# Performance work log

Measured on AMD Instinct MI355X. Metric: run time of the kernel, lower is better.

The kernel has to match this reference:

```python
import jax, jax.numpy as jnp
import numpy as np

B, T, C, H, N = 2, 1024, 2048, 32, 64
KVH = 8                       # GQA kv heads
KV = KVH * N                  # 512
REP = H // KVH                # 4
EPS = 1e-6
LORA = [96, 96, 64, 256, 64]  # xw, xa, xv, xg, xk lora dims


def rmsnorm(x, w, eps=EPS):
    xf = x.astype(jnp.float32)
    var = jnp.mean(xf * xf, axis=-1, keepdims=True)
    return (w * (xf * jax.lax.rsqrt(var + eps))).astype(x.dtype)


def rotate_half(x):
    x1, x2 = jnp.split(x, 2, axis=-1)
    return jnp.concatenate([-x2, x1], axis=-1)


def rwkv7_scan(r, w, k, v, a, b, state0):
    # r,w,k,v,a,b: [B,T,H,N]; state0: [B,H,N,N] (value x key)
    # per step: S = S*exp(w) + (S@a) b^T + v k^T ; o = S @ r
    def step(S, inp):
        r_t, w_t, k_t, v_t, a_t, b_t = inp  # each [B,H,N]
        sa = jnp.einsum('bhvk,bhk->bhv', S, a_t)
        S = (S * jnp.exp(w_t)[:, :, None, :]
             + sa[..., None] * b_t[:, :, None, :]
             + v_t[..., None] * k_t[:, :, None, :])
        o = jnp.einsum('bhvk,bhk->bhv', S, r_t)
        return S, o
    seqs = tuple(jnp.moveaxis(t, 1, 0) for t in (r, w, k, v, a, b))
    S, o = jax.lax.scan(step, state0, seqs)
    return jnp.moveaxis(o, 0, 1), S


def setup_inputs() -> dict:
    key = jax.random.key(0)
    ks = jax.random.split(key, 24)
    g = lambda i, shape, s=0.02: jax.random.normal(ks[i], shape, jnp.float32) * s
    # real rope cache, theta = 1e6, rotary_dim = N
    pos = jnp.arange(T, dtype=jnp.float32)
    inv = 1.0 / (1e6 ** (jnp.arange(0, N, 2, dtype=jnp.float32) / N))
    ang = pos[:, None] * inv[None, :]
    ang = jnp.concatenate([ang, ang], axis=-1)  # [T, N]
    cos = jnp.broadcast_to(jnp.cos(ang)[None], (B, T, N))
    sin = jnp.broadcast_to(jnp.sin(ang)[None], (B, T, N))
    return dict(
        x_in=jax.random.normal(ks[0], (B, T, C), jnp.float32),
        v_first=jax.random.normal(ks[1], (B, T, KVH, N), jnp.float32),
        k_first=jax.random.normal(ks[2], (B, T, KVH, N), jnp.float32),
        state=jnp.zeros((B, H, N, N), jnp.float32),
        calc_cos=cos, calc_sin=sin,
        ln1=jnp.ones((C,), jnp.float32), ln2=jnp.ones((C,), jnp.float32),
        ln_r=jnp.ones((N,), jnp.float32), ln_k=jnp.ones((N,), jnp.float32),
        wavgk1=g(3, (C, sum(LORA))),
        w0=g(4, (H * N,)), w2=g(5, (LORA[0], H * N)),
        a0=g(6, (H * N,)), a2=g(7, (LORA[1], H * N)),
        v0=g(8, (KV,)), v2=g(9, (LORA[2], KV)),
        k0=g(10, (KV,)), k2=g(11, (LORA[4], KV)),
        g2=g(12, (LORA[3], H * N)),
        r_k=g(13, (H, N)),
        RKV_W=g(14, (C, H * N + 2 * KV)),
        O_W=g(15, (H * N, C)),
        R_bias=g(16, (H * N,)), K_bias=g(17, (KV,)), V_bias=g(18, (KV,)),
    )


def _forward(x_in, v_first, k_first, state, calc_cos, calc_sin,
             ln1, ln2, ln_r, ln_k, wavgk1, w0, w2, a0, a2, v0, v2,
             k0, k2, g2, r_k, RKV_W, O_W, R_bias, K_bias, V_bias):
    x = rmsnorm(x_in, ln1)
    xw, xa, xv, xg, xk = jnp.split(x @ wavgk1, np.cumsum(LORA)[:-1].tolist(), axis=-1)
    r, k, v = jnp.split(x @ RKV_W, [H * N, H * N + KV], axis=-1)
    r = (r + R_bias).reshape(B, T, H, N)
    k = (k + K_bias).reshape(B, T, KVH, N)
    v = (v + V_bias).reshape(B, T, KVH, N)
    r = rmsnorm(r, ln_r)
    k = rmsnorm(k, ln_k)
    cos = calc_cos[:, :, None, :]
    sin = calc_sin[:, :, None, :]
    r = r * cos + rotate_half(r) * sin
    k = k * cos + rotate_half(k) * sin
    # layer_id != 0: sigmoid-gated interpolation toward first-layer v/k
    v = v + (v_first - v) * jax.nn.sigmoid(xv @ v2 + v0).reshape(B, T, KVH, N)
    k = k + (k_first - k) * jax.nn.sigmoid(xk @ k2 + k0).reshape(B, T, KVH, N)
    # GQA repeat (contiguous per kv head, as repeat_kv does)
    k = jnp.repeat(k, REP, axis=2).reshape(B, T, H * N)
    v = jnp.repeat(v, REP, axis=2).reshape(B, T, H * N)
    a = jax.nn.sigmoid(xa @ a2 + a0)
    kh = k.reshape(B, T, H, N)
    kk = (kh / (jnp.linalg.norm(kh, axis=-1, keepdims=True) + 1e-12)).reshape(B, T, H * N)
    w = jnp.tanh(xw) @ w2 + w0
    w = -jax.nn.softplus(-w) - 0.5
    k = k * (1.0 - w + a)
    aa = -kk
    bb = kk * a
    wlog = -jnp.exp(w)
    sh = (B, T, H, N)
    o, state = rwkv7_scan(r, wlog.reshape(sh), k.reshape(sh), v.reshape(sh),
                          aa.reshape(sh), bb.reshape(sh), state)
    xx = o.reshape(B, T, H * N) * (float(N) ** -0.5)
    bonus = ((r * k.reshape(sh) * r_k).sum(axis=-1, keepdims=True)
             * v.reshape(sh)).reshape(B, T, H * N)
    xx = xx + bonus
    out = (xx * (jax.nn.sigmoid(xg) @ g2)) @ O_W
    x_res = x_in + out
    output = rmsnorm(x_res, ln2)
    return output, x[:, -1], state, v_first, k_first, x_res


def reference(x_in, v_first, k_first, state, calc_cos, calc_sin,
              ln1, ln2, ln_r, ln_k, wavgk1, w0, w2, a0, a2, v0, v2,
              k0, k2, g2, r_k, RKV_W, O_W, R_bias, K_bias, V_bias):
    return _forward(x_in, v_first, k_first, state, calc_cos, calc_sin,
                    ln1, ln2, ln_r, ln_k, wavgk1, w0, w2, a0, a2, v0, v2,
                    k0, k2, g2, r_k, RKV_W, O_W, R_bias, K_bias, V_bias)
```

## Files before the change

### kernel.cpp

```cpp
#include <hip/hip_runtime.h>
#include <hip/hip_bf16.h>

#define BT 2
#define TT 1024
#define CC 2048
#define HH 32
#define MM (BT*TT)
#define TCH 512
#define NCH (TT/TCH)
#define RECB 896

typedef __attribute__((ext_vector_type(8))) short short8;
typedef __attribute__((ext_vector_type(4))) float floatx4;
typedef __attribute__((ext_vector_type(2))) float f32x2;

static __device__ __forceinline__ float bf2f(__hip_bfloat16 x){ return __bfloat162float(x); }
static __device__ __forceinline__ __hip_bfloat16 f2bf(float x){ return __float2bfloat16(x); }
static __device__ __forceinline__ float sigm(float x){ return 1.0f/(1.0f + expf(-x)); }
static __device__ __forceinline__ float u2f(unsigned short u){
  union { unsigned int i; float f; } x; x.i = ((unsigned int)u) << 16; return x.f;
}
static __device__ __forceinline__ float ulo(unsigned int u){ return __uint_as_float(u << 16); }
static __device__ __forceinline__ float uhi(unsigned int u){ return __uint_as_float(u & 0xffff0000u); }
static __device__ __forceinline__ unsigned short bfbits(float x){
  __hip_bfloat16 h = f2bf(x);
  unsigned short s; __builtin_memcpy(&s, &h, 2); return s;
}
static __device__ __forceinline__ unsigned int pkbf(float lo, float hi){
  return (unsigned int)bfbits(lo) | ((unsigned int)bfbits(hi) << 16);
}

#if defined(__has_builtin)
#if __has_builtin(__builtin_amdgcn_global_load_lds)
#define HAVE_GLL 1
#endif
#endif

#ifdef HAVE_GLL
static __device__ __forceinline__ void gll16(const void* g, void* l){
  __builtin_amdgcn_global_load_lds(
      (__attribute__((address_space(1))) void*)const_cast<void*>(g),
      (__attribute__((address_space(3))) void*)l,
      16, 0, 0);
}
#endif

#define DPP_ADD(x, ctrl) ((x) + __int_as_float(__builtin_amdgcn_update_dpp(0, __float_as_int(x), (ctrl), 0xF, 0xF, true)))

#if defined(__has_builtin)
#if __has_builtin(__builtin_amdgcn_permlane16_swap) && __has_builtin(__builtin_amdgcn_permlane32_swap)
#define HAVE_PLSWAP 1
#endif
#endif

#ifdef HAVE_PLSWAP
typedef unsigned int uint2v __attribute__((ext_vector_type(2)));
static __device__ __forceinline__ float row16_pair_add(float x){
  unsigned int u = __float_as_uint(x);
  uint2v r = __builtin_amdgcn_permlane16_swap(u, u, false, false);
  return __uint_as_float(r[0]) + __uint_as_float(r[1]);
}
static __device__ __forceinline__ float half32_pair_add(float x){
  unsigned int u = __float_as_uint(x);
  uint2v r = __builtin_amdgcn_permlane32_swap(u, u, false, false);
  return __uint_as_float(r[0]) + __uint_as_float(r[1]);
}
#else
static __device__ __forceinline__ float row16_pair_add(float x){ return x + __shfl_xor(x, 16); }
static __device__ __forceinline__ float half32_pair_add(float x){ return x + __shfl_xor(x, 32); }
#endif

static __device__ __forceinline__ float red8(float x){
  x = DPP_ADD(x, 0xB1);
  x = DPP_ADD(x, 0x4E);
  x = DPP_ADD(x, 0x141);
  return x;
}
static __device__ __forceinline__ float red32(float x){
  x = DPP_ADD(x, 0xB1);
  x = DPP_ADD(x, 0x4E);
  x = DPP_ADD(x, 0x124);
  x = DPP_ADD(x, 0x128);
  return row16_pair_add(x);
}
static __device__ __forceinline__ float red64(float x){
  x = DPP_ADD(x, 0xB1);
  x = DPP_ADD(x, 0x4E);
  x = DPP_ADD(x, 0x124);
  x = DPP_ADD(x, 0x128);
  x = row16_pair_add(x);
  return half32_pair_add(x);
}

__global__ __launch_bounds__(256) void tcvt_kernel(
    const float* __restrict__ W, __hip_bfloat16* __restrict__ Wt,
    int K, int N, int Npad)
{
  __shared__ float tile[32][33];
  const int bn = blockIdx.x*32, bk = blockIdx.y*32;
  const int tx = threadIdx.x & 31, ty0 = threadIdx.x >> 5;
#pragma unroll
  for (int i=0;i<4;++i){
    const int kk = bk + ty0 + i*8;
    float val = 0.f;
    if (kk < K && bn + tx < N) val = W[(size_t)kk*N + bn + tx];
    tile[ty0 + i*8][tx] = val;
  }
  __syncthreads();
#pragma unroll
  for (int i=0;i<4;++i){
    const int nn = bn + ty0 + i*8;
    const int kk = bk + tx;
    if (nn < Npad && kk < K) Wt[(size_t)nn*K + kk] = f2bf(tile[tx][ty0 + i*8]);
  }
}

__global__ __launch_bounds__(256) void rmsnorm1_kernel(
    const float* __restrict__ x_in,
    const float* __restrict__ ln1,
    __hip_bfloat16* __restrict__ x_bf,
    float* __restrict__ x_last)
{
  const int m = blockIdx.x;
  const int tid = threadIdx.x;
  const int c = tid * 8;
  const float* xp = x_in + (size_t)m*CC + c;
  float v[8]; float ss = 0.f;
#pragma unroll
  for (int i=0;i<8;++i){ v[i] = xp[i]; ss += v[i]*v[i]; }
  ss = red64(ss);
  __shared__ float wsum[4];
  if ((tid&63)==0) wsum[tid>>6] = ss;
  __syncthreads();
  ss = wsum[0]+wsum[1]+wsum[2]+wsum[3];
  const float sc = rsqrtf(ss * (1.0f/CC) + 1e-6f);
#pragma unroll
  for (int i=0;i<8;++i) {
    const float y = ln1[c+i] * v[i] * sc;
    x_bf[(size_t)m*CC + c + i] = f2bf(y);
    if ((m % TT) == TT-1) x_last[(size_t)(m/TT)*CC + c + i] = y;
  }
}

template<bool F32OUT, int ACT>
__global__ __launch_bounds__(256) void mgemm(
    const __hip_bfloat16* __restrict__ A, int lda,
    const __hip_bfloat16* __restrict__ Bt,
    void* __restrict__ C, int N, int K)
{
  __shared__ __align__(16) short As[128*32];
  __shared__ __align__(16) short Bs[128*32];
  const int tid = threadIdx.x;
  const int bm = blockIdx.x * 128;
  const int bn = blockIdx.y * 128;
  const int wid = tid >> 6;
  const int lane = tid & 63;
  const int m16 = lane & 15, quad = lane >> 4;
  const int wm = wid & 1, wn = wid >> 1;
  const int lrow = tid >> 2;
  const int lcol = (tid & 3) * 8;

  floatx4 acc[4][4];
#pragma unroll
  for (int i=0;i<4;++i)
#pragma unroll
    for (int j=0;j<4;++j) acc[i][j] = (floatx4){0.f,0.f,0.f,0.f};

  char* asl = (char*)As + tid*16;
  char* bsl = (char*)Bs + tid*16;

  for (int k0 = 0; k0 < K; k0 += 32) {
    __syncthreads();
#ifdef HAVE_GLL
    gll16(A  + (size_t)(bm + lrow)      * lda + k0 + lcol, asl);
    gll16(A  + (size_t)(bm + 64 + lrow) * lda + k0 + lcol, asl + 4096);
    gll16(Bt + (size_t)(bn + lrow)      * K   + k0 + lcol, bsl);
    gll16(Bt + (size_t)(bn + 64 + lrow) * K   + k0 + lcol, bsl + 4096);
#else
    uint4 a0v = *(const uint4*)(const void*)(A  + (size_t)(bm + lrow)      * lda + k0 + lcol);
    uint4 a1v = *(const uint4*)(const void*)(A  + (size_t)(bm + 64 + lrow) * lda + k0 + lcol);
    uint4 b0v = *(const uint4*)(const void*)(Bt + (size_t)(bn + lrow)      * K   + k0 + lcol);
    uint4 b1v = *(const uint4*)(const void*)(Bt + (size_t)(bn + 64 + lrow) * K   + k0 + lcol);
    *(uint4*)(void*)(asl)        = a0v;
    *(uint4*)(void*)(asl + 4096) = a1v;
    *(uint4*)(void*)(bsl)        = b0v;
    *(uint4*)(void*)(bsl + 4096) = b1v;
#endif
    __syncthreads();

    short8 af[4], bfg[4];
#pragma unroll
    for (int mi=0; mi<4; ++mi)
      af[mi] = *(const short8*)(const void*)(As + (wm*64 + mi*16 + m16)*32 + quad*8);
#pragma unroll
    for (int ni=0; ni<4; ++ni)
      bfg[ni] = *(const short8*)(const void*)(Bs + (wn*64 + ni*16 + m16)*32 + quad*8);
#pragma unroll
    for (int mi=0; mi<4; ++mi)
#pragma unroll
      for (int ni=0; ni<4; ++ni)
        acc[mi][ni] = __builtin_amdgcn_mfma_f32_16x16x32_bf16(af[mi], bfg[ni], acc[mi][ni], 0,0,0);
  }

#pragma unroll
  for (int mi=0; mi<4; ++mi) {
    const int row = bm + wm*64 + mi*16 + quad*4;
#pragma unroll
    for (int ni=0; ni<4; ++ni) {
      const int col = bn + wn*64 + ni*16 + m16;
      if (col < N) {
        if (F32OUT) {
          float* cp = (float*)C;
#pragma unroll
          for (int r=0;r<4;++r) cp[(size_t)(row+r)*N + col] = acc[mi][ni][r];
        } else {
          __hip_bfloat16* cp = (__hip_bfloat16*)C;
#pragma unroll
          for (int r=0;r<4;++r) {
            float x = acc[mi][ni][r];
            if (ACT == 1) {
              if (col < 96) x = tanhf(x);
              else if (col >= 256 && col < 512) x = sigm(x);
            }
            cp[(size_t)(row+r)*N + col] = f2bf(x);
          }
        }
      }
    }
  }
}

__global__ __launch_bounds__(256) void prep_kernel(
    const __hip_bfloat16* __restrict__ RKV,
    const __hip_bfloat16* __restrict__ Wpre,
    const __hip_bfloat16* __restrict__ Apre,
    const __hip_bfloat16* __restrict__ Vsig,
    const __hip_bfloat16* __restrict__ Ksig,
    const float* __restrict__ v_first,
    const float* __restrict__ k_first,
    const float* __restrict__ cosp,
    const float* __restrict__ sinp,
    const float* __restrict__ ln_r,
    const float* __restrict__ ln_k,
    const float* __restrict__ r_k,
    const float* __restrict__ w0,
    const float* __restrict__ a0,
    const float* __restrict__ v0,
    const float* __restrict__ k0b,
    const float* __restrict__ R_bias,
    const float* __restrict__ K_bias,
    const float* __restrict__ V_bias,
    char* __restrict__ rec,
    float* __restrict__ bonus,
    int t0)
{
  const int b    = blockIdx.x / TCH;
  const int tloc = blockIdx.x % TCH;
  const int t    = t0 + tloc;
  const int m    = b*TT + t;
  const int tid = threadIdx.x;
  const int h  = tid >> 3;
  const int j  = tid & 7;
  const int hk = h >> 2;
  const int nb = j * 8;
  const int hn = h*64 + nb;
  const int kn = hk*64 + nb;

  const size_t rbase = (size_t)m*3072 + h*64 + nb;
  const size_t kbase = (size_t)m*3072 + 2048 + kn;
  const size_t vbase = kbase + 512;

  float r[8], k[8], v[8];
  float ssr = 0.f, ssk = 0.f;
#pragma unroll
  for (int i=0;i<8;++i) {
    r[i] = bf2f(RKV[rbase+i]) + R_bias[hn+i];
    k[i] = bf2f(RKV[kbase+i]) + K_bias[kn+i];
    v[i] = bf2f(RKV[vbase+i]) + V_bias[kn+i];
    ssr += r[i]*r[i];
    ssk += k[i]*k[i];
  }
  ssr = red8(ssr);
  ssk = red8(ssk);
  const float scr = rsqrtf(ssr*(1.0f/64.0f) + 1e-6f);
  const float sck = rsqrtf(ssk*(1.0f/64.0f) + 1e-6f);
#pragma unroll
  for (int i=0;i<8;++i) {
    r[i] = ln_r[nb+i] * r[i] * scr;
    k[i] = ln_k[nb+i] * k[i] * sck;
  }
  const float sgn = (j < 4) ? -1.0f : 1.0f;
  float rr[8], kr[8];
#pragma unroll
  for (int i=0;i<8;++i) {
    const float cs = cosp[(size_t)m*64 + nb + i];
    const float sn = sinp[(size_t)m*64 + nb + i];
    const float pr = __shfl_xor(r[i], 4);
    const float pk = __shfl_xor(k[i], 4);
    rr[i] = r[i]*cs + sgn*pr*sn;
    kr[i] = k[i]*cs + sgn*pk*sn;
  }
  float av[8], ew[8], wv2[8];
  float ssn = 0.f;
#pragma unroll
  for (int i=0;i<8;++i) {
    const float vs = sigm(bf2f(Vsig[(size_t)m*512 + kn + i]) + v0[kn+i]);
    v[i]  = v[i]  + (v_first[(size_t)m*512 + kn + i] - v[i])  * vs;
    const float ks = sigm(bf2f(Ksig[(size_t)m*512 + kn + i]) + k0b[kn+i]);
    kr[i] = kr[i] + (k_first[(size_t)m*512 + kn + i] - kr[i]) * ks;
    ssn += kr[i]*kr[i];
    av[i] = sigm(bf2f(Apre[(size_t)m*2048 + hn + i]) + a0[hn+i]);
    float wraw = bf2f(Wpre[(size_t)m*2048 + hn + i]) + w0[hn+i];
    const float xs = -wraw;
    const float sp = fmaxf(xs, 0.f) + log1pf(expf(-fabsf(xs)));
    const float wv = -sp - 0.5f;
    wv2[i] = wv;
    ew[i] = expf(-expf(wv));
  }
  ssn = red8(ssn);
  const float inrm = 1.0f / (sqrtf(ssn) + 1e-12f);
  float kf[8], kkv[8];
  float bsum = 0.f;
#pragma unroll
  for (int i=0;i<8;++i) {
    kkv[i] = kr[i] * inrm;
    kf[i]  = kr[i] * (1.0f - wv2[i] + av[i]);
    bsum  += rr[i] * kf[i] * r_k[hn+i];
  }
  bsum = red8(bsum);

  char* base = rec + ((size_t)(b*HH + h)*TCH + tloc)*RECB;
  const int klb = nb >> 1;
#pragma unroll
  for (int p=0;p<4;++p) {
    const int i0 = 2*p, i1 = i0 + 1;
    uint4 Aw;
    Aw.x = __float_as_uint(ew[i0]);
    Aw.y = __float_as_uint(ew[i1]);
    Aw.z = pkbf(rr[i0], rr[i1]);
    Aw.w = pkbf(kf[i0], kf[i1]);
    *(uint4*)(void*)(base + (size_t)(klb + p)*16) = Aw;
    uint2 Bw;
    Bw.x = pkbf(kkv[i0], kkv[i1]);
    Bw.y = pkbf(-kkv[i0]*av[i0], -kkv[i1]*av[i1]);
    *(uint2*)(void*)(base + 512 + (size_t)(klb + p)*8) = Bw;
  }
  short8 vs8;
#pragma unroll
  for (int i=0;i<8;++i) vs8[i] = (short)bfbits(v[i]);
  *(short8*)(void*)(base + 768 + (size_t)nb*2) = vs8;
#pragma unroll
  for (int i=0;i<8;++i)
    bonus[(size_t)m*2048 + hn + i] = bsum * v[i];
}

__global__ __launch_bounds__(256) void scan_kernel(
    const char* __restrict__ rec,
    float* __restrict__ state,
    float* __restrict__ o_out,
    int t0)
{
  const int blk = blockIdx.x;
  const int bh  = blk & 63;
  const int q   = blk >> 6;
  const int b   = bh >> 5, h = bh & 31;
  const int tid = threadIdx.x;
  const int vl  = q*8 + (tid >> 5);
  const int kl  = tid & 31;
  const int k2  = kl*2;

  const char* base = rec + (size_t)bh * TCH * RECB;
  float* sp = state + ((size_t)bh*64 + vl)*64 + k2;
  f32x2 S; S.x = sp[0]; S.y = sp[1];

  const char* pA = base + kl*16;
  const char* pB = base + 512 + kl*8;
  const char* pv = base + 768 + vl*2;

  uint4 Ab[4]; uint2 Bb[4]; unsigned short vb[4];
#pragma unroll
  for (int s=0;s<4;++s){
    Ab[s] = *(const uint4*)(const void*)(pA + s*RECB);
    Bb[s] = *(const uint2*)(const void*)(pB + s*RECB);
    vb[s] = *(const unsigned short*)(const void*)(pv + s*RECB);
  }
  pA += 4*RECB; pB += 4*RECB; pv += 4*RECB;

  int oidx = (b*TT + t0)*CC + h*64 + vl - CC;
  float opart = 0.f;

#define SCAN_STEP(jj, PF, ST)                                                  \
  {                                                                            \
    const uint4 A  = Ab[jj];                                                   \
    const uint2 Bv = Bb[jj];                                                   \
    const float vf = u2f(vb[jj]);                                              \
    if (PF) {                                                                  \
      Ab[jj] = *(const uint4*)(const void*)(pA + jj*RECB);                     \
      Bb[jj] = *(const uint2*)(const void*)(pB + jj*RECB);                     \
      vb[jj] = *(const unsigned short*)(const void*)(pv + jj*RECB);            \
    }                                                                          \
    float op = red32(opart);                                                   \
    f32x2 kk; kk.x = ulo(Bv.x); kk.y = uhi(Bv.x);                              \
    const f32x2 prod = S * kk;                                                 \
    float sa = prod.x + prod.y;                                                \
    sa = red32(sa);                                                            \
    if (ST && kl == 0) o_out[oidx] = op;                                       \
    f32x2 ew; ew.x = __uint_as_float(A.x); ew.y = __uint_as_float(A.y);        \
    f32x2 bb; bb.x = ulo(Bv.y); bb.y = uhi(Bv.y);                              \
    f32x2 kf; kf.x = ulo(A.w); kf.y = uhi(A.w);                                \
    f32x2 sav; sav.x = sa; sav.y = sa;                                         \
    f32x2 vfv; vfv.x = vf; vfv.y = vf;                                         \
    S = S*ew + sav*bb + vfv*kf;                                                \
    f32x2 rv; rv.x = ulo(A.z); rv.y = uhi(A.z);                                \
    const f32x2 ov = S * rv;                                                   \
    opart = ov.x + ov.y;                                                       \
    oidx += CC;                                                                \
  }

  SCAN_STEP(0, true, 0)
  SCAN_STEP(1, true, 1)
  SCAN_STEP(2, true, 1)
  SCAN_STEP(3, true, 1)
  pA += 4*RECB; pB += 4*RECB; pv += 4*RECB;

  for (int t = 4; t < TCH-4; t += 4) {
    SCAN_STEP(0, true, 1)
    SCAN_STEP(1, true, 1)
    SCAN_STEP(2, true, 1)
    SCAN_STEP(3, true, 1)
    pA += 4*RECB; pB += 4*RECB; pv += 4*RECB;
  }
  SCAN_STEP(0, false, 1)
  SCAN_STEP(1, false, 1)
  SCAN_STEP(2, false, 1)
  SCAN_STEP(3, false, 1)
#undef SCAN_STEP

  opart = red32(opart);
  if (kl == 0)
    o_out[oidx] = opart;

  sp[0]=S.x; sp[1]=S.y;
}

__global__ void xxg_kernel(const float* __restrict__ o_in,
                           const float* __restrict__ bonus,
                           const __hip_bfloat16* __restrict__ G,
                           __hip_bfloat16* __restrict__ xxg)
{
  int i = blockIdx.x*256 + threadIdx.x;
  xxg[i] = f2bf((o_in[i]*0.125f + bonus[i]) * bf2f(G[i]));
}

__global__ __launch_bounds__(256) void final_kernel(
    const float* __restrict__ x_in,
    const float* __restrict__ OUTb,
    const float* __restrict__ ln2,
    float* __restrict__ seg0,
    float* __restrict__ seg5)
{
  const int m = blockIdx.x;
  const int tid = threadIdx.x;
  const int c = tid*8;
  const float* xp = x_in + (size_t)m*CC + c;
  const float* op = OUTb + (size_t)m*CC + c;
  float xr[8]; float ss = 0.f;
#pragma unroll
  for (int i=0;i<8;++i){ xr[i] = xp[i] + op[i]; ss += xr[i]*xr[i]; }
#pragma unroll
  for (int i=0;i<8;++i) seg5[(size_t)m*CC + c + i] = xr[i];
  ss = red64(ss);
  __shared__ float wsum[4];
  if ((tid&63)==0) wsum[tid>>6] = ss;
  __syncthreads();
  ss = wsum[0]+wsum[1]+wsum[2]+wsum[3];
  const float sc = rsqrtf(ss*(1.0f/CC) + 1e-6f);
#pragma unroll
  for (int i=0;i<8;++i) seg0[(size_t)m*CC + c + i] = ln2[c+i] * xr[i] * sc;
}

extern "C" void kernel_launch(void* const* d_in, const int* in_sizes, int n_in,
                              void* d_out, int out_size, void* d_ws, size_t ws_size,
                              hipStream_t stream)
{
  (void)in_sizes; (void)n_in; (void)out_size; (void)ws_size;
  const float* x_in   = (const float*)d_in[0];
  const float* v_first= (const float*)d_in[1];
  const float* k_first= (const float*)d_in[2];
  const float* state0 = (const float*)d_in[3];
  const float* cosp   = (const float*)d_in[4];
  const float* sinp   = (const float*)d_in[5];
  const float* ln1    = (const float*)d_in[6];
  const float* ln2    = (const float*)d_in[7];
  const float* ln_r   = (const float*)d_in[8];
  const float* ln_k   = (const float*)d_in[9];
  const float* wavgk1 = (const float*)d_in[10];
  const float* w0     = (const float*)d_in[11];
  const float* w2     = (const float*)d_in[12];
  const float* a0     = (const float*)d_in[13];
  const float* a2     = (const float*)d_in[14];
  const float* v0     = (const float*)d_in[15];
  const float* v2     = (const float*)d_in[16];
  const float* k0b    = (const float*)d_in[17];
  const float* k2     = (const float*)d_in[18];
  const float* g2     = (const float*)d_in[19];
  const float* r_k    = (const float*)d_in[20];
  const float* RKV_W  = (const float*)d_in[21];
  const float* O_W    = (const float*)d_in[22];
  const float* R_bias = (const float*)d_in[23];
  const float* K_bias = (const float*)d_in[24];
  const float* V_bias = (const float*)d_in[25];

  float* out  = (float*)d_out;
  float* seg0 = out;
  float* seg1 = out + 4194304;
  float* seg2 = out + 4198400;
  float* seg3 = out + 4460544;
  float* seg4 = out + 5509120;
  float* seg5 = out + 6557696;

  char* ws = (char*)d_ws;
  const size_t OFF_STF   = 0;
  const size_t OFF_OWT   = 1048576;
  const size_t OFF_G     = 9437184;
  const size_t OFF_VSIG  = 17825792;
  const size_t OFF_KSIG  = 19922944;
  const size_t OFF_WPRE  = 22020096;
  const size_t OFF_APRE  = 30408704;
  const size_t OFF_RKV   = 38797312;
  const size_t OFF_XBF   = 51380224;
  const size_t OFF_Y1    = 59768832;
  const size_t OFF_WT    = 62128128;
  const size_t OFF_WAVT  = OFF_WT;
  const size_t OFF_RKVT  = OFF_WAVT + 2621440;
  const size_t OFF_W2T   = OFF_RKVT + 12582912;
  const size_t OFF_A2T   = OFF_W2T  + 393216;
  const size_t OFF_V2T   = OFF_A2T  + 393216;
  const size_t OFF_K2T   = OFF_V2T  + 65536;
  const size_t OFF_G2T   = OFF_K2T  + 65536;
  const size_t OFF_REC   = OFF_WT;
  const size_t OFF_XXG   = OFF_XBF;
  const size_t OFF_OUT   = OFF_WPRE;

  float*          stf   = (float*)(ws + OFF_STF);
  __hip_bfloat16* owt   = (__hip_bfloat16*)(ws + OFF_OWT);
  __hip_bfloat16* Gbuf  = (__hip_bfloat16*)(ws + OFF_G);
  __hip_bfloat16* Vsig  = (__hip_bfloat16*)(ws + OFF_VSIG);
  __hip_bfloat16* Ksig  = (__hip_bfloat16*)(ws + OFF_KSIG);
  __hip_bfloat16* Wpre  = (__hip_bfloat16*)(ws + OFF_WPRE);
  __hip_bfloat16* Apre  = (__hip_bfloat16*)(ws + OFF_APRE);
  __hip_bfloat16* RKV   = (__hip_bfloat16*)(ws + OFF_RKV);
  __hip_bfloat16* x_bf  = (__hip_bfloat16*)(ws + OFF_XBF);
  __hip_bfloat16* Y1    = (__hip_bfloat16*)(ws + OFF_Y1);
  __hip_bfloat16* wavt  = (__hip_bfloat16*)(ws + OFF_WAVT);
  __hip_bfloat16* rkvt  = (__hip_bfloat16*)(ws + OFF_RKVT);
  __hip_bfloat16* w2t   = (__hip_bfloat16*)(ws + OFF_W2T);
  __hip_bfloat16* a2t   = (__hip_bfloat16*)(ws + OFF_A2T);
  __hip_bfloat16* v2t   = (__hip_bfloat16*)(ws + OFF_V2T);
  __hip_bfloat16* k2t   = (__hip_bfloat16*)(ws + OFF_K2T);
  __hip_bfloat16* g2t   = (__hip_bfloat16*)(ws + OFF_G2T);
  char*           rec   = ws + OFF_REC;
  __hip_bfloat16* xxg   = (__hip_bfloat16*)(ws + OFF_XXG);
  float*          OUTb  = (float*)(ws + OFF_OUT);

  float* o_st = seg0;
  float* b_st = seg5;

  tcvt_kernel<<<dim3(20, 64), 256, 0, stream>>>(wavgk1, wavt, 2048, 576, 640);
  tcvt_kernel<<<dim3(96, 64), 256, 0, stream>>>(RKV_W,  rkvt, 2048, 3072, 3072);
  tcvt_kernel<<<dim3(64, 64), 256, 0, stream>>>(O_W,    owt,  2048, 2048, 2048);
  tcvt_kernel<<<dim3(64,  3), 256, 0, stream>>>(w2,     w2t,    96, 2048, 2048);
  tcvt_kernel<<<dim3(64,  3), 256, 0, stream>>>(a2,     a2t,    96, 2048, 2048);
  tcvt_kernel<<<dim3(16,  2), 256, 0, stream>>>(v2,     v2t,    64,  512,  512);
  tcvt_kernel<<<dim3(16,  2), 256, 0, stream>>>(k2,     k2t,    64,  512,  512);
  tcvt_kernel<<<dim3(64,  8), 256, 0, stream>>>(g2,     g2t,   256, 2048, 2048);

  rmsnorm1_kernel<<<MM, 256, 0, stream>>>(x_in, ln1, x_bf, seg1);
  mgemm<false,1><<<dim3(16,  5), 256, 0, stream>>>(x_bf, CC, wavt, Y1,   576, 2048);
  mgemm<false,0><<<dim3(16, 24), 256, 0, stream>>>(x_bf, CC, rkvt, RKV, 3072, 2048);
  mgemm<false,0><<<dim3(16, 16), 256, 0, stream>>>(Y1+0,   576, w2t, Wpre, 2048, 96);
  mgemm<false,0><<<dim3(16, 16), 256, 0, stream>>>(Y1+96,  576, a2t, Apre, 2048, 96);
  mgemm<false,0><<<dim3(16,  4), 256, 0, stream>>>(Y1+192, 576, v2t, Vsig,  512, 64);
  mgemm<false,0><<<dim3(16,  4), 256, 0, stream>>>(Y1+512, 576, k2t, Ksig,  512, 64);
  mgemm<false,0><<<dim3(16, 16), 256, 0, stream>>>(Y1+256, 576, g2t, Gbuf, 2048, 256);

  hipMemcpyAsync(stf, state0, (size_t)1048576, hipMemcpyDeviceToDevice, stream);
  for (int c = 0; c < NCH; ++c) {
    const int t0 = c*TCH;
    prep_kernel<<<BT*TCH, 256, 0, stream>>>(RKV, Wpre, Apre, Vsig, Ksig, v_first, k_first,
                                            cosp, sinp, ln_r, ln_k, r_k, w0, a0, v0, k0b,
                                            R_bias, K_bias, V_bias, rec, b_st, t0);
    scan_kernel<<<BT*HH*8, 256, 0, stream>>>(rec, stf, o_st, t0);
  }
  hipMemcpyAsync(seg2, stf, (size_t)1048576, hipMemcpyDeviceToDevice, stream);

  xxg_kernel<<<(MM*CC)/256, 256, 0, stream>>>(o_st, b_st, Gbuf, xxg);
  mgemm<true,0><<<dim3(16, 16), 256, 0, stream>>>(xxg, CC, owt, OUTb, 2048, 2048);
  final_kernel<<<MM, 256, 0, stream>>>(x_in, OUTb, ln2, seg0, seg5);

  hipMemcpyAsync(seg3, v_first, (size_t)1048576*4, hipMemcpyDeviceToDevice, stream);
  hipMemcpyAsync(seg4, k_first, (size_t)1048576*4, hipMemcpyDeviceToDevice, stream);
}
```

Baseline: 664.8 us.

## Scan with one state element per lane and repack records into 12-byte key entries

Each scan thread now owns a single state element (64 lanes per value row, 4 rows per block) instead of two, and the grid doubles to 16 blocks per head. The per-step record layout is repacked from separate 16-byte and 8-byte segments per key pair into one 12-byte entry per key, holding decay, packed r/kf, and packed kk/bb. The goal is to spread the serial recurrence over more wavefronts and halve per-thread ALU work per step. In exchange each reduction now spans the full 64-lane wavefront with a cross-half step, and the 12-byte unaligned loads may be less efficient.

```diff
diff --git a/kernel.cpp b/kernel.cpp
--- a/kernel.cpp
+++ b/kernel.cpp
@@ -12,7 +12,6 @@
 
 typedef __attribute__((ext_vector_type(8))) short short8;
 typedef __attribute__((ext_vector_type(4))) float floatx4;
-typedef __attribute__((ext_vector_type(2))) float f32x2;
 
 static __device__ __forceinline__ float bf2f(__hip_bfloat16 x){ return __bfloat162float(x); }
 static __device__ __forceinline__ __hip_bfloat16 f2bf(float x){ return __float2bfloat16(x); }
@@ -29,6 +28,8 @@
 static __device__ __forceinline__ unsigned int pkbf(float lo, float hi){
   return (unsigned int)bfbits(lo) | ((unsigned int)bfbits(hi) << 16);
 }
+
+struct u32x3 { unsigned int x, y, z; };
 
 #if defined(__has_builtin)
 #if __has_builtin(__builtin_amdgcn_global_load_lds)
@@ -75,13 +76,6 @@
   x = DPP_ADD(x, 0x4E);
   x = DPP_ADD(x, 0x141);
   return x;
-}
-static __device__ __forceinline__ float red32(float x){
-  x = DPP_ADD(x, 0xB1);
-  x = DPP_ADD(x, 0x4E);
-  x = DPP_ADD(x, 0x124);
-  x = DPP_ADD(x, 0x128);
-  return row16_pair_add(x);
 }
 static __device__ __forceinline__ float red64(float x){
   x = DPP_ADD(x, 0xB1);
@@ -330,20 +324,13 @@
   bsum = red8(bsum);
 
   char* base = rec + ((size_t)(b*HH + h)*TCH + tloc)*RECB;
-  const int klb = nb >> 1;
-#pragma unroll
-  for (int p=0;p<4;++p) {
-    const int i0 = 2*p, i1 = i0 + 1;
-    uint4 Aw;
-    Aw.x = __float_as_uint(ew[i0]);
-    Aw.y = __float_as_uint(ew[i1]);
-    Aw.z = pkbf(rr[i0], rr[i1]);
-    Aw.w = pkbf(kf[i0], kf[i1]);
-    *(uint4*)(void*)(base + (size_t)(klb + p)*16) = Aw;
-    uint2 Bw;
-    Bw.x = pkbf(kkv[i0], kkv[i1]);
-    Bw.y = pkbf(-kkv[i0]*av[i0], -kkv[i1]*av[i1]);
-    *(uint2*)(void*)(base + 512 + (size_t)(klb + p)*8) = Bw;
+#pragma unroll
+  for (int i=0;i<8;++i) {
+    u32x3 w;
+    w.x = __float_as_uint(ew[i]);
+    w.y = pkbf(rr[i], kf[i]);
+    w.z = pkbf(kkv[i], -kkv[i]*av[i]);
+    *(u32x3*)(void*)(base + (size_t)(nb + i)*12) = w;
   }
   short8 vs8;
 #pragma unroll
@@ -365,55 +352,41 @@
   const int q   = blk >> 6;
   const int b   = bh >> 5, h = bh & 31;
   const int tid = threadIdx.x;
-  const int vl  = q*8 + (tid >> 5);
-  const int kl  = tid & 31;
-  const int k2  = kl*2;
+  const int vl  = q*4 + (tid >> 6);
+  const int kl  = tid & 63;
 
   const char* base = rec + (size_t)bh * TCH * RECB;
-  float* sp = state + ((size_t)bh*64 + vl)*64 + k2;
-  f32x2 S; S.x = sp[0]; S.y = sp[1];
-
-  const char* pA = base + kl*16;
-  const char* pB = base + 512 + kl*8;
+  float* sp = state + ((size_t)bh*64 + vl)*64 + kl;
+  float S = sp[0];
+
+  const char* pA = base + kl*12;
   const char* pv = base + 768 + vl*2;
 
-  uint4 Ab[4]; uint2 Bb[4]; unsigned short vb[4];
+  u32x3 Ab[4]; unsigned short vb[4];
 #pragma unroll
   for (int s=0;s<4;++s){
-    Ab[s] = *(const uint4*)(const void*)(pA + s*RECB);
-    Bb[s] = *(const uint2*)(const void*)(pB + s*RECB);
+    Ab[s] = *(const u32x3*)(const void*)(pA + s*RECB);
     vb[s] = *(const unsigned short*)(const void*)(pv + s*RECB);
   }
-  pA += 4*RECB; pB += 4*RECB; pv += 4*RECB;
+  pA += 4*RECB; pv += 4*RECB;
 
   int oidx = (b*TT + t0)*CC + h*64 + vl - CC;
   float opart = 0.f;
 
 #define SCAN_STEP(jj, PF, ST)                                                  \
   {                                                                            \
-    const uint4 A  = Ab[jj];                                                   \
-    const uint2 Bv = Bb[jj];                                                   \
+    const u32x3 A  = Ab[jj];                                                   \
     const float vf = u2f(vb[jj]);                                              \
     if (PF) {                                                                  \
-      Ab[jj] = *(const uint4*)(const void*)(pA + jj*RECB);                     \
-      Bb[jj] = *(const uint2*)(const void*)(pB + jj*RECB);                     \
+      Ab[jj] = *(const u32x3*)(const void*)(pA + jj*RECB);                     \
       vb[jj] = *(const unsigned short*)(const void*)(pv + jj*RECB);            \
     }                                                                          \
-    float op = red32(opart);                                                   \
-    f32x2 kk; kk.x = ulo(Bv.x); kk.y = uhi(Bv.x);                              \
-    const f32x2 prod = S * kk;                                                 \
-    float sa = prod.x + prod.y;                                                \
-    sa = red32(sa);                                                            \
+    float op = red64(opart);                                                   \
+    const float kk = ulo(A.z);                                                 \
+    float sa = red64(S * kk);                                                  \
     if (ST && kl == 0) o_out[oidx] = op;                                       \
-    f32x2 ew; ew.x = __uint_as_float(A.x); ew.y = __uint_as_float(A.y);        \
-    f32x2 bb; bb.x = ulo(Bv.y); bb.y = uhi(Bv.y);                              \
-    f32x2 kf; kf.x = ulo(A.w); kf.y = uhi(A.w);                                \
-    f32x2 sav; sav.x = sa; sav.y = sa;                                         \
-    f32x2 vfv; vfv.x = vf; vfv.y = vf;                                         \
-    S = S*ew + sav*bb + vfv*kf;                                                \
-    f32x2 rv; rv.x = ulo(A.z); rv.y = uhi(A.z);                                \
-    const f32x2 ov = S * rv;                                                   \
-    opart = ov.x + ov.y;                                                       \
+    S = S*__uint_as_float(A.x) + sa*uhi(A.z) + vf*uhi(A.y);                    \
+    opart = S * ulo(A.y);                                                      \
     oidx += CC;                                                                \
   }
 
@@ -421,14 +394,14 @@
   SCAN_STEP(1, true, 1)
   SCAN_STEP(2, true, 1)
   SCAN_STEP(3, true, 1)
-  pA += 4*RECB; pB += 4*RECB; pv += 4*RECB;
+  pA += 4*RECB; pv += 4*RECB;
 
   for (int t = 4; t < TCH-4; t += 4) {
     SCAN_STEP(0, true, 1)
     SCAN_STEP(1, true, 1)
     SCAN_STEP(2, true, 1)
     SCAN_STEP(3, true, 1)
-    pA += 4*RECB; pB += 4*RECB; pv += 4*RECB;
+    pA += 4*RECB; pv += 4*RECB;
   }
   SCAN_STEP(0, false, 1)
   SCAN_STEP(1, false, 1)
@@ -436,11 +409,11 @@
   SCAN_STEP(3, false, 1)
 #undef SCAN_STEP
 
-  opart = red32(opart);
+  opart = red64(opart);
   if (kl == 0)
     o_out[oidx] = opart;
 
-  sp[0]=S.x; sp[1]=S.y;
+  sp[0] = S;
 }
 
 __global__ void xxg_kernel(const float* __restrict__ o_in,
@@ -590,7 +563,7 @@
     prep_kernel<<<BT*TCH, 256, 0, stream>>>(RKV, Wpre, Apre, Vsig, Ksig, v_first, k_first,
                                             cosp, sinp, ln_r, ln_k, r_k, w0, a0, v0, k0b,
                                             R_bias, K_bias, V_bias, rec, b_st, t0);
-    scan_kernel<<<BT*HH*8, 256, 0, stream>>>(rec, stf, o_st, t0);
+    scan_kernel<<<BT*HH*16, 256, 0, stream>>>(rec, stf, o_st, t0);
   }
   hipMemcpyAsync(seg2, stf, (size_t)1048576, hipMemcpyDeviceToDevice, stream);
 
```

After: 762.8 us. 1.15x slower.
